# Kernel tuning notes

Measured on AMD Instinct MI355X. Metric: run time of the kernel, lower is better.

The kernel has to match this reference:

```python
import jax, jax.numpy as jnp
import numpy as np
from jax import lax

# config (matches init_kwargs)
NUM_CLASSES = 10
SCORE_THRESH = 0.05
TOPK = 1000
DET_PER_IMG = 100
NMS_SCORE = 0.3
NMS_SIGMA = 0.5
IMG_H, IMG_W = 800.0, 1333.0
IOU_SUPPRESS = 0.8
BBOX_XFORM_CLIP = float(np.log(1000.0 / 16.0))
EPS = 1e-7


def setup_inputs() -> dict:
    key = jax.random.key(0)
    k1, k2, k3 = jax.random.split(key, 3)
    B, A, C = 8, 200000, NUM_CLASSES
    cls_logits = jax.random.normal(k1, (B, A, C), dtype=jnp.float32)
    bbox_regression = 0.5 * jax.random.normal(k2, (B, A, 4), dtype=jnp.float32)
    # plausible anchors: random centers + sizes inside the image, xyxy format
    u = jax.random.uniform(k3, (A, 6), dtype=jnp.float32)
    cx = u[:, 0] * IMG_W
    cy = u[:, 1] * IMG_H
    w = 16.0 + u[:, 2] * 200.0
    h = 16.0 + u[:, 3] * 200.0
    anchors = jnp.stack([cx - 0.5 * w, cy - 0.5 * h, cx + 0.5 * w, cy + 0.5 * h], axis=-1)
    return {"cls_logits": cls_logits, "bbox_regression": bbox_regression, "anchors": anchors}


def _decode(rel, anc):
    # torchvision BoxCoder.decode_single, weights (1,1,1,1). rel, anc: [K,4] xyxy anchors
    wa = anc[:, 2] - anc[:, 0]
    ha = anc[:, 3] - anc[:, 1]
    cxa = anc[:, 0] + 0.5 * wa
    cya = anc[:, 1] + 0.5 * ha
    dx, dy = rel[:, 0], rel[:, 1]
    dw = jnp.minimum(rel[:, 2], BBOX_XFORM_CLIP)
    dh = jnp.minimum(rel[:, 3], BBOX_XFORM_CLIP)
    cx = dx * wa + cxa
    cy = dy * ha + cya
    w = jnp.exp(dw) * wa
    h = jnp.exp(dh) * ha
    boxes = jnp.stack([cx - 0.5 * w, cy - 0.5 * h, cx + 0.5 * w, cy + 0.5 * h], axis=-1)
    # clip_boxes_to_image
    x = jnp.clip(boxes[:, 0::2], 0.0, IMG_W)
    y = jnp.clip(boxes[:, 1::2], 0.0, IMG_H)
    return jnp.stack([x[:, 0], y[:, 0], x[:, 1], y[:, 1]], axis=-1)


def _iou_one(box, boxes):
    # box [4] vs boxes [K,4] -> [K]
    lt = jnp.maximum(box[:2], boxes[:, :2])
    rb = jnp.minimum(box[2:], boxes[:, 2:])
    wh = jnp.clip(rb - lt, 0.0)
    inter = wh[:, 0] * wh[:, 1]
    a1 = (box[2] - box[0]) * (box[3] - box[1])
    a2 = (boxes[:, 2] - boxes[:, 0]) * (boxes[:, 3] - boxes[:, 1])
    return inter / (a1 + a2 - inter + EPS)


def _postprocess_one(logits, rel, anchors):
    # logits [A,C], rel [A,4], anchors [A,4]
    probs = jax.nn.sigmoid(logits)
    scores_all = jnp.max(probs, axis=-1)               # [A]
    labels_all = jnp.argmax(probs, axis=-1)            # [A]
    scores_all = jnp.where(scores_all > SCORE_THRESH, scores_all, 0.0)
    top_scores, top_idx = lax.top_k(scores_all, TOPK)  # [K]
    labels = labels_all[top_idx]
    boxes = _decode(rel[top_idx], anchors[top_idx])    # [K,4]

    K = TOPK
    # --- batched gaussian soft-NMS (same-label decay only) ---
    def soft_step(carry, _):
        sc, out = carry
        i = jnp.argmax(sc)
        s = sc[i]
        out = out.at[i].set(jnp.maximum(s, 0.0))
        ious = _iou_one(boxes[i], boxes)
        decay = jnp.where(labels == labels[i], jnp.exp(-(ious ** 2) / NMS_SIGMA), 1.0)
        sc = (sc * decay).at[i].set(-1.0)
        return (sc, out), None
    (_, decayed), _ = lax.scan(soft_step, (top_scores, jnp.zeros_like(top_scores)), None, length=K)
    keep = decayed > NMS_SCORE

    # --- sort by decayed score desc, greedy hard suppression at IoU>0.8 ---
    order = jnp.argsort(-decayed)
    b = boxes[order]
    s = decayed[order]
    l = labels[order]
    alive0 = keep[order]
    idxs = jnp.arange(K)

    def greedy_step(alive, i):
        ious = _iou_one(b[i], b)
        suppress = (ious > IOU_SUPPRESS) & (idxs > i)
        alive = jnp.where(alive[i], alive & ~suppress, alive)
        return alive, None
    alive, _ = lax.scan(greedy_step, alive0, idxs)

    final_scores = jnp.where(alive, s, -1.0)
    out_scores, out_i = lax.top_k(final_scores, DET_PER_IMG)  # preserves desc order of survivors
    return b[out_i], out_scores, l[out_i]


def reference(cls_logits, bbox_regression, anchors):
    boxes, scores, labels = jax.vmap(_postprocess_one, in_axes=(0, 0, None))(
        cls_logits, bbox_regression, anchors)
    return boxes, scores, labels  # [B,D,4], [B,D], [B,D] (score -1 = padding)
```

## Files before the change

kernel.cpp:

```cpp
#include <hip/hip_runtime.h>
#include <math.h>

#define NCLS 10
#define TOPK 1000
#define DETS 100
#define CANDMAX 4096
#define SLOTS 16
#define ACTK 256
#define TILE 256

#define NB2 256
#define MGATE (-2.9444389791664403f)
#define SEAM 2.2f
#define SCA 30.907200f
#define SCB 41.0f
#define NBLKB 256

__device__ __forceinline__ float sigmoidf_(float x) {
    return 1.0f / (1.0f + expf(-x));
}

__device__ __forceinline__ int mbin_(float m) {
    if (!(m > MGATE)) return 0;
    int b;
    if (m > SEAM) { b = 161 + (int)((m - SEAM) * SCB); if (b > 255) b = 255; }
    else          { b = 1 + (int)((m - MGATE) * SCA);  if (b > 160) b = 160; }
    return b;
}

__device__ __forceinline__ float key_score(const unsigned long long* key, int c) {
    return __uint_as_float(~(unsigned)(key[c] >> 32));
}

__device__ __forceinline__ unsigned fkey_(float f) {
    unsigned b = __float_as_uint(f);
    return (b & 0x80000000u) ? ~b : (b | 0x80000000u);
}
__device__ __forceinline__ float funkey_(unsigned k) {
    return __uint_as_float((k & 0x80000000u) ? (k & 0x7FFFFFFFu) : ~k);
}

__device__ __forceinline__ unsigned wave_umax_(unsigned x) {
    unsigned t;
    t = (unsigned)__builtin_amdgcn_update_dpp(0, (int)x, 0x111, 0xF, 0xF, false); x = (x > t) ? x : t;
    t = (unsigned)__builtin_amdgcn_update_dpp(0, (int)x, 0x112, 0xF, 0xF, false); x = (x > t) ? x : t;
    t = (unsigned)__builtin_amdgcn_update_dpp(0, (int)x, 0x114, 0xF, 0xF, false); x = (x > t) ? x : t;
    t = (unsigned)__builtin_amdgcn_update_dpp(0, (int)x, 0x118, 0xF, 0xF, false); x = (x > t) ? x : t;
    t = (unsigned)__builtin_amdgcn_update_dpp(0, (int)x, 0x142, 0xF, 0xF, false); x = (x > t) ? x : t;
    t = (unsigned)__builtin_amdgcn_update_dpp(0, (int)x, 0x143, 0xF, 0xF, false); x = (x > t) ? x : t;
    return (unsigned)__builtin_amdgcn_readlane((int)x, 63);
}

__global__ __launch_bounds__(256) void k_score_bins(const float* __restrict__ logits,
                                                    unsigned char* __restrict__ binc,
                                                    unsigned* hist,
                                                    unsigned* __restrict__ done,
                                                    unsigned* __restrict__ P,
                                                    int A) {
    __shared__ float tilef[TILE * NCLS];
    __shared__ unsigned h[4][NB2];
    __shared__ int s_last;
    int img = blockIdx.y;
    int tid = threadIdx.x;
    for (int i = tid; i < 4 * NB2; i += 256) ((unsigned*)h)[i] = 0;
    __syncthreads();

    const float* base = logits + (size_t)img * A * NCLS;
    unsigned char* bc = binc + (size_t)img * A;
    int rep = tid & 3;

    int ntile = A / TILE;
    for (int tile = blockIdx.x; tile < ntile; tile += NBLKB) {
        const float4* src = (const float4*)(base + (size_t)tile * TILE * NCLS);
        float4 v0 = src[tid];
        float4 v1 = src[256 + tid];
        float4 v2;
        if (tid < 128) v2 = src[512 + tid];
        ((float4*)tilef)[tid] = v0;
        ((float4*)tilef)[256 + tid] = v1;
        if (tid < 128) ((float4*)tilef)[512 + tid] = v2;
        __syncthreads();
        float m = tilef[tid * 10];
#pragma unroll
        for (int c = 1; c < 10; ++c) m = fmaxf(m, tilef[tid * 10 + c]);
        int b = mbin_(m);
        bc[(size_t)tile * TILE + tid] = (unsigned char)b;
        if (b) atomicAdd(&h[rep][b], 1u);
        __syncthreads();
    }
    if (blockIdx.x == 0) {
        for (int a = ntile * TILE + tid; a < A; a += 256) {
            const float* lp2 = base + (size_t)a * NCLS;
            float m = lp2[0];
            for (int c = 1; c < 10; ++c) m = fmaxf(m, lp2[c]);
            int b = mbin_(m);
            bc[a] = (unsigned char)b;
            if (b) atomicAdd(&h[rep][b], 1u);
        }
    }
    __syncthreads();
    for (int i = tid; i < NB2; i += 256) {
        unsigned c = h[0][i] + h[1][i] + h[2][i] + h[3][i];
        if (c) atomicAdd(&hist[(size_t)img * NB2 + i], c);
    }
    __syncthreads();
    if (tid == 0) {
        __threadfence();
        unsigned old = atomicAdd(&done[img], 1u);
        s_last = (old == (unsigned)(NBLKB - 1)) ? 1 : 0;
    }
    __syncthreads();
    if (s_last && tid < 64) {
        int lane = tid;
        unsigned* hh = hist + (size_t)img * NB2;
        unsigned b4[4];
        unsigned s = 0;
#pragma unroll
        for (int j = 0; j < 4; ++j) { b4[j] = atomicAdd(&hh[lane * 4 + j], 0u); s += b4[j]; }
        unsigned suf = s;
#pragma unroll
        for (int d = 1; d < 64; d <<= 1) {
            unsigned o = __shfl_down(suf, d);
            if (lane + d < 64) suf += o;
        }
        unsigned above = __shfl_down(suf, 1);
        if (lane == 63) above = 0;
        if (lane == 0 && suf < (unsigned)TOPK) P[img] = 0u;
        if (above < (unsigned)TOPK && suf >= (unsigned)TOPK) {
            unsigned cum = above;
            for (int j = 3; j >= 0; --j) {
                cum += b4[j];
                if (cum >= (unsigned)TOPK) { P[img] = (unsigned)(lane * 4 + j); break; }
            }
        }
    }
}

__global__ __launch_bounds__(1024) void k_sortnms(const unsigned char* __restrict__ binc,
                                                  const unsigned* __restrict__ P,
                                                  const float* __restrict__ logits,
                                                  const float* __restrict__ rel,
                                                  const float* __restrict__ anch,
                                                  float* __restrict__ out, int A, int B) {
    __shared__ unsigned long long key[CANDMAX];
    __shared__ float s_box[TOPK][4];
    __shared__ int   s_lab[TOPK];
    __shared__ float s_pbox[TOPK][4];
    __shared__ int   s_plab[TOPK];
    __shared__ float s_psc[TOPK];
    __shared__ int   s_alive[TOPK];
    __shared__ unsigned s_n;

    const float CLIPV = 4.135166556742356f;
    const float EPS = 1e-7f;
    const float W_ = 1333.0f, H_ = 800.0f;

    int img = blockIdx.x;
    int tid = threadIdx.x;
    const float* base = logits + (size_t)img * A * NCLS;

    if (tid == 0) s_n = 0;
    __syncthreads();
    {
        unsigned p = P[img];
        unsigned psel = p ? (p - 1u) : 0u;
        const unsigned* b4 = (const unsigned*)(binc + (size_t)img * A);
        int nquad = A >> 2;
        int nq4 = nquad >> 2;
        for (int g = tid; g < nq4; g += 1024) {
            uint4 u = ((const uint4*)b4)[g];
            unsigned ws[4] = {u.x, u.y, u.z, u.w};
#pragma unroll
            for (int w2 = 0; w2 < 4; ++w2) {
                unsigned ub = ws[w2];
#pragma unroll
                for (int j = 0; j < 4; ++j) {
                    unsigned bj = (ub >> (8 * j)) & 0xFFu;
                    if ((psel == 0u) || (bj >= psel)) {
                        unsigned pos = atomicAdd(&s_n, 1u);
                        if (pos < CANDMAX)
                            key[pos] = (unsigned long long)(unsigned)((g * 4 + w2) * 4 + j);
                    }
                }
            }
        }
        for (int q = (nq4 << 2) + tid; q < nquad; q += 1024) {
            unsigned ub = b4[q];
#pragma unroll
            for (int j = 0; j < 4; ++j) {
                unsigned bj = (ub >> (8 * j)) & 0xFFu;
                if ((psel == 0u) || (bj >= psel)) {
                    unsigned pos = atomicAdd(&s_n, 1u);
                    if (pos < CANDMAX)
                        key[pos] = (unsigned long long)(unsigned)(q * 4 + j);
                }
            }
        }
        for (int a = (nquad << 2) + tid; a < A; a += 1024) {
            unsigned bj = binc[(size_t)img * A + a];
            if ((psel == 0u) || (bj >= psel)) {
                unsigned pos = atomicAdd(&s_n, 1u);
                if (pos < CANDMAX)
                    key[pos] = (unsigned long long)(unsigned)a;
            }
        }
    }
    __syncthreads();
    unsigned n = s_n;
    if (n > CANDMAX) n = CANDMAX;
    int L = (n <= 1024) ? 1024 : (n <= 2048) ? 2048 : CANDMAX;

    for (int t2 = tid; t2 < (int)n; t2 += 1024) {
        unsigned a = (unsigned)key[t2];
        const float* lp = base + (size_t)a * NCLS;
        float m = lp[0];
#pragma unroll
        for (int c = 1; c < 10; ++c) m = fmaxf(m, lp[c]);
        float sc = sigmoidf_(m);
        sc = (sc > 0.05f) ? sc : 0.0f;
        unsigned bits = __float_as_uint(sc);
        key[t2] = ((unsigned long long)(~bits) << 32) | a;
    }
    for (int i = (int)n + tid; i < CANDMAX; i += 1024) key[i] = ~0ull;
    __syncthreads();

    for (int k = 2; k <= L; k <<= 1) {
        for (int j = k >> 1; j > 0; j >>= 1) {
            for (int i = tid; i < L; i += 1024) {
                int l = i ^ j;
                if (l > i) {
                    unsigned long long va = key[i], vb = key[l];
                    bool up = ((i & k) == 0);
                    if (up ? (va > vb) : (va < vb)) { key[i] = vb; key[l] = va; }
                }
            }
            __syncthreads();
        }
    }

    if (tid < TOPK) {
        unsigned long long ik = key[tid];
        unsigned ai = (unsigned)ik;
        if (ai >= (unsigned)A) ai = 0;
        const float* lp = base + (size_t)ai * NCLS;
        float best = sigmoidf_(lp[0]); int lbb = 0;
#pragma unroll
        for (int cc = 1; cc < NCLS; ++cc) {
            float v = sigmoidf_(lp[cc]);
            if (v > best) { best = v; lbb = cc; }
        }
        const float* rp = rel + ((size_t)img * A + ai) * 4;
        const float* ap = anch + (size_t)ai * 4;
        float a0 = ap[0], a1 = ap[1], a2 = ap[2], a3 = ap[3];
        float wa = a2 - a0, ha = a3 - a1;
        float cxa = a0 + 0.5f * wa, cya = a1 + 0.5f * ha;
        float dx = rp[0], dy = rp[1];
        float dw = fminf(rp[2], CLIPV), dh = fminf(rp[3], CLIPV);
        float cx = dx * wa + cxa, cy = dy * ha + cya;
        float w = expf(dw) * wa, h = expf(dh) * ha;
        s_box[tid][0] = fminf(fmaxf(cx - 0.5f * w, 0.0f), W_);
        s_box[tid][1] = fminf(fmaxf(cy - 0.5f * h, 0.0f), H_);
        s_box[tid][2] = fminf(fmaxf(cx + 0.5f * w, 0.0f), W_);
        s_box[tid][3] = fminf(fmaxf(cy + 0.5f * h, 0.0f), H_);
        s_lab[tid] = lbb;
    }
    __syncthreads();
    if (tid >= 64) return;
    int lane = tid;

    int M = TOPK;
    int need_full = 0;
    float bound = key_score(key, ACTK);

    {
        float sc[4], x1[4], y1[4], x2[4], y2[4], ar[4];
        int lb[4];
#pragma unroll
        for (int j = 0; j < 4; ++j) {
            int c = lane + (j << 6);
            float4 bb = *(const float4*)&s_box[c][0];
            x1[j] = bb.x; y1[j] = bb.y; x2[j] = bb.z; y2[j] = bb.w;
            ar[j] = (bb.z - bb.x) * (bb.w - bb.y);
            lb[j] = s_lab[c];
            sc[j] = key_score(key, c);
        }

        int nconf = 0, Mf = -1;

        for (int t = 0; t < ACTK; ++t) {
            float bv = sc[0]; int bj = 0;
#pragma unroll
            for (int j = 1; j < 4; ++j)
                if (sc[j] > bv) { bv = sc[j]; bj = j; }
            unsigned mk = fkey_(bv);
            unsigned mx = wave_umax_(mk);
            float pcur = funkey_(mx);

            if (!(pcur >= bound)) { need_full = 1; break; }

            int pick = -1;
#pragma unroll
            for (int jj = 0; jj < 4; ++jj) {
                if (pick < 0) {
                    unsigned long long mj = __ballot(mk == mx && bj == jj);
                    if (mj) pick = (jj << 6) + (__ffsll(mj) - 1);
                }
            }

            float psc = fmaxf(pcur, 0.0f);
            float4 pb = *(const float4*)&s_box[pick][0];
            int plab_ = s_lab[pick];
            if (lane == 0) {
                *(float4*)&s_pbox[t][0] = pb;
                s_plab[t] = plab_;
                s_psc[t] = psc;
            }

            float4 qb[4]; int ga[4];
#pragma unroll
            for (int k = 0; k < 4; ++k) {
                int p = lane + (k << 6);
                int pc2 = (p < t) ? p : 0;
                qb[k] = *(const float4*)&s_pbox[pc2][0];
                ga[k] = (p < t) ? s_alive[pc2] : 0;
            }

            float wax = (pb.z - pb.x) * (pb.w - pb.y);
#pragma unroll
            for (int j = 0; j < 4; ++j) {
                float lx2 = fmaxf(pb.x, x1[j]), ly2 = fmaxf(pb.y, y1[j]);
                float rx2 = fminf(pb.z, x2[j]), ry2 = fminf(pb.w, y2[j]);
                float iw2 = fmaxf(rx2 - lx2, 0.0f), ih2 = fmaxf(ry2 - ly2, 0.0f);
                float inter2 = iw2 * ih2;
                bool hot = (inter2 > 0.0f) && (lb[j] == plab_);
                if (__ballot(hot) != 0ull) {
                    float iou2 = inter2 / (wax + ar[j] - inter2 + EPS);
                    float ie = (lb[j] == plab_) ? iou2 : 0.0f;
                    sc[j] *= expf(-(ie * ie) / 0.5f);
                }
            }
#pragma unroll
            for (int j = 0; j < 4; ++j)
                if (lane + (j << 6) == pick) sc[j] = -1.0f;

            bool sup = false;
#pragma unroll
            for (int k = 0; k < 4; ++k) {
                if (ga[k]) {
                    float lx = fmaxf(pb.x, qb[k].x), ly = fmaxf(pb.y, qb[k].y);
                    float rx = fminf(pb.z, qb[k].z), ry = fminf(pb.w, qb[k].w);
                    float iw = fmaxf(rx - lx, 0.0f), ih = fmaxf(ry - ly, 0.0f);
                    float inter = iw * ih;
                    float qa = (qb[k].z - qb[k].x) * (qb[k].w - qb[k].y);
                    float iou = inter / (wax + qa - inter + EPS);
                    sup = sup || (iou > 0.8f);
                }
            }
            bool alive = (psc > 0.3f) && (__ballot(sup) == 0ull);
            if (lane == 0) s_alive[t] = alive ? 1 : 0;
            nconf += alive ? 1 : 0;
            if (nconf >= DETS) { Mf = t + 1; break; }
        }
        if (!need_full) {
            if (Mf < 0) need_full = 1;
            else M = Mf;
        }
    }

    if (need_full) {
        float sc[SLOTS], x1[SLOTS], y1[SLOTS], x2[SLOTS], y2[SLOTS], ar[SLOTS];
        int lb[SLOTS];
#pragma unroll
        for (int j = 0; j < SLOTS; ++j) {
            int c = lane + (j << 6);
            if (c < TOPK) {
                float4 bb = *(const float4*)&s_box[c][0];
                x1[j] = bb.x; y1[j] = bb.y; x2[j] = bb.z; y2[j] = bb.w;
                ar[j] = (bb.z - bb.x) * (bb.w - bb.y);
                lb[j] = s_lab[c];
                sc[j] = key_score(key, c);
            } else {
                sc[j] = -2.0f; lb[j] = -1;
                x1[j] = y1[j] = x2[j] = y2[j] = ar[j] = 0.0f;
            }
        }
        unsigned long long aw = 0;
        if (lane < 15) aw = ~0ull;
        else if (lane == 15) aw = (1ull << (TOPK - 15 * 64)) - 1;
        int f = 0, nconf = 0;
        M = TOPK;
        for (int t = 0; t < TOPK; ++t) {
            int fp = (f < TOPK) ? f : 0;
            float4 fb = *(const float4*)&s_box[fp][0];
            int flab = s_lab[fp];
            int fs = f >> 6;
            float v = sc[0];
#pragma unroll
            for (int j = 1; j < SLOTS; ++j) if (fs == j) v = sc[j];
            float cf = __shfl(v, f & 63);
            float lm = sc[0];
#pragma unroll
            for (int j = 1; j < SLOTS; ++j) lm = fmaxf(lm, sc[j]);
            int pick; float pcur; float4 pb; int plab_;
            unsigned long long bb2 = __ballot(lm > cf);
            if (bb2 == 0) {
                pick = f; pcur = cf; pb = fb; plab_ = flab;
            } else {
                float bv = sc[0]; int bi = lane;
#pragma unroll
                for (int j = 1; j < SLOTS; ++j) {
                    int e = lane + (j << 6);
                    if (sc[j] > bv) { bv = sc[j]; bi = e; }
                }
#pragma unroll
                for (int d = 32; d; d >>= 1) {
                    float ov = __shfl_xor(bv, d);
                    int oi = __shfl_xor(bi, d);
                    if (ov > bv || (ov == bv && oi < bi)) { bv = ov; bi = oi; }
                }
                pick = bi; pcur = bv;
                pb = *(const float4*)&s_box[pick][0];
                plab_ = s_lab[pick];
            }
            float psc = fmaxf(pcur, 0.0f);
            if (lane == 0) {
                *(float4*)&s_pbox[t][0] = pb;
                s_plab[t] = plab_;
                s_psc[t] = psc;
            }
            bool alive = (psc > 0.3f);
            if (alive && t > 0) {
                float pa = (pb.z - pb.x) * (pb.w - pb.y);
                int kprev = ((t - 1) >> 6) + 1;
                bool sup = false;
                for (int k = 0; k < kprev; ++k) {
                    int p = lane + (k << 6);
                    int pc = (p < t) ? p : 0;
                    float4 qb = *(const float4*)&s_pbox[pc][0];
                    int ga = s_alive[pc];
                    if (p < t && ga) {
                        float lx = fmaxf(pb.x, qb.x), ly = fmaxf(pb.y, qb.y);
                        float rx = fminf(pb.z, qb.z), ry = fminf(pb.w, qb.w);
                        float iw = fmaxf(rx - lx, 0.0f), ih = fmaxf(ry - ly, 0.0f);
                        float inter = iw * ih;
                        float qa = (qb.z - qb.x) * (qb.w - qb.y);
                        float iou = inter / (pa + qa - inter + EPS);
                        sup = sup || (iou > 0.8f);
                    }
                }
                alive = (__ballot(sup) == 0ull);
            }
            if (lane == 0) s_alive[t] = alive ? 1 : 0;
            nconf += alive ? 1 : 0;
            if (nconf >= DETS) { M = t + 1; break; }
            float wax = (pb.z - pb.x) * (pb.w - pb.y);
#pragma unroll
            for (int j = 0; j < SLOTS; ++j) {
                float lx2 = fmaxf(pb.x, x1[j]), ly2 = fmaxf(pb.y, y1[j]);
                float rx2 = fminf(pb.z, x2[j]), ry2 = fminf(pb.w, y2[j]);
                float iw2 = fmaxf(rx2 - lx2, 0.0f), ih2 = fmaxf(ry2 - ly2, 0.0f);
                float inter2 = iw2 * ih2;
                bool hot = (inter2 > 0.0f) && (lb[j] == plab_);
                if (__ballot(hot) != 0ull) {
                    float iou2 = inter2 / (wax + ar[j] - inter2 + EPS);
                    float ie = (lb[j] == plab_) ? iou2 : 0.0f;
                    sc[j] *= expf(-(ie * ie) / 0.5f);
                }
            }
#pragma unroll
            for (int j = 0; j < SLOTS; ++j)
                if (lane + (j << 6) == pick) sc[j] = -1.0f;
            if (lane == (pick >> 6)) aw &= ~(1ull << (pick & 63));
            if (pick == f) {
                int fw = f >> 6;
                unsigned long long w2 = __shfl(aw, fw);
                while (w2 == 0ull && fw < 15) { ++fw; w2 = __shfl(aw, fw); }
                f = (w2 == 0ull) ? TOPK : (fw << 6) + (__ffsll(w2) - 1);
            }
        }
    }

    float* out_boxes  = out;
    float* out_scores = out + (size_t)B * DETS * 4;
    float* out_labels = out + (size_t)B * DETS * 5;
    int kmax = (M + 63) >> 6;
    int base2 = 0;
    for (int k = 0; k < kmax; ++k) {
        int p = lane + (k << 6);
        bool av = (p < M) && (s_alive[p] != 0);
        unsigned long long mask = __ballot(av);
        int slot = base2 + (int)__popcll(mask & ((1ull << lane) - 1ull));
        if (av && slot < DETS) {
            float4 pb = *(const float4*)&s_pbox[p][0];
            float* ob = out_boxes + ((size_t)img * DETS + slot) * 4;
            ob[0] = pb.x; ob[1] = pb.y; ob[2] = pb.z; ob[3] = pb.w;
            out_scores[img * DETS + slot] = s_psc[p];
            out_labels[img * DETS + slot] = (float)s_plab[p];
        }
        base2 += (int)__popcll(mask);
    }
    if (base2 < DETS) {
        int dbase = 0;
        for (int k = 0; k < kmax; ++k) {
            int p = lane + (k << 6);
            bool dd = (p < M) && (s_alive[p] == 0);
            unsigned long long mask = __ballot(dd);
            int slot = base2 + dbase + (int)__popcll(mask & ((1ull << lane) - 1ull));
            if (dd && slot < DETS) {
                float4 pb = *(const float4*)&s_pbox[p][0];
                float* ob = out_boxes + ((size_t)img * DETS + slot) * 4;
                ob[0] = pb.x; ob[1] = pb.y; ob[2] = pb.z; ob[3] = pb.w;
                out_scores[img * DETS + slot] = -1.0f;
                out_labels[img * DETS + slot] = (float)s_plab[p];
            }
            dbase += (int)__popcll(mask);
        }
    }
}

extern "C" void kernel_launch(void* const* d_in, const int* in_sizes, int n_in,
                              void* d_out, int out_size, void* d_ws, size_t ws_size,
                              hipStream_t stream) {
    const float* logits = (const float*)d_in[0];
    const float* rel = (const float*)d_in[1];
    const float* anch = (const float*)d_in[2];
    float* out = (float*)d_out;

    int A = in_sizes[2] / 4;
    int B = in_sizes[0] / (A * NCLS);

    char* w = (char*)d_ws;
    unsigned* hist = (unsigned*)w;           w += (size_t)B * NB2 * 4;
    unsigned* done = (unsigned*)w;           w += (size_t)B * 4;
    size_t zbytes = (size_t)(w - (char*)d_ws);
    unsigned* P = (unsigned*)w;              w += (size_t)B * 4;
    unsigned char* binc = (unsigned char*)w;

    hipMemsetAsync(d_ws, 0, zbytes, stream);

    dim3 g1(NBLKB, (unsigned)B);
    k_score_bins<<<g1, 256, 0, stream>>>(logits, binc, hist, done, P, A);
    k_sortnms<<<B, 1024, 0, stream>>>(binc, P, logits, rel, anch, out, A, B);
}
```

Baseline: 226.6 us.

## Drop LDS tiling in score-bin pass and skip intra-wave bitonic barriers

```diff
diff --git a/kernel.cpp b/kernel.cpp
--- a/kernel.cpp
+++ b/kernel.cpp
@@ -7,7 +7,6 @@
 #define CANDMAX 4096
 #define SLOTS 16
 #define ACTK 256
-#define TILE 256
 
 #define NB2 256
 #define MGATE (-2.9444389791664403f)
@@ -57,7 +56,6 @@
                                                     unsigned* __restrict__ done,
                                                     unsigned* __restrict__ P,
                                                     int A) {
-    __shared__ float tilef[TILE * NCLS];
     __shared__ unsigned h[4][NB2];
     __shared__ int s_last;
     int img = blockIdx.y;
@@ -69,27 +67,26 @@
     unsigned char* bc = binc + (size_t)img * A;
     int rep = tid & 3;
 
-    int ntile = A / TILE;
-    for (int tile = blockIdx.x; tile < ntile; tile += NBLKB) {
-        const float4* src = (const float4*)(base + (size_t)tile * TILE * NCLS);
-        float4 v0 = src[tid];
-        float4 v1 = src[256 + tid];
-        float4 v2;
-        if (tid < 128) v2 = src[512 + tid];
-        ((float4*)tilef)[tid] = v0;
-        ((float4*)tilef)[256 + tid] = v1;
-        if (tid < 128) ((float4*)tilef)[512 + tid] = v2;
-        __syncthreads();
-        float m = tilef[tid * 10];
-#pragma unroll
-        for (int c = 1; c < 10; ++c) m = fmaxf(m, tilef[tid * 10 + c]);
-        int b = mbin_(m);
-        bc[(size_t)tile * TILE + tid] = (unsigned char)b;
-        if (b) atomicAdd(&h[rep][b], 1u);
-        __syncthreads();
+    int nquad = A >> 2;
+    for (int q = blockIdx.x * 256 + tid; q < nquad; q += NBLKB * 256) {
+        const float4* lp = (const float4*)(base + (size_t)q * 40);
+        float f[40];
+#pragma unroll
+        for (int i = 0; i < 10; ++i) ((float4*)f)[i] = lp[i];
+        unsigned ub = 0;
+#pragma unroll
+        for (int j = 0; j < 4; ++j) {
+            float m = f[10 * j];
+#pragma unroll
+            for (int c = 1; c < 10; ++c) m = fmaxf(m, f[10 * j + c]);
+            int b = mbin_(m);
+            ub |= ((unsigned)b) << (8 * j);
+            if (b) atomicAdd(&h[rep][b], 1u);
+        }
+        *(unsigned*)(bc + (size_t)q * 4) = ub;
     }
     if (blockIdx.x == 0) {
-        for (int a = ntile * TILE + tid; a < A; a += 256) {
+        for (int a = (nquad << 2) + tid; a < A; a += 256) {
             const float* lp2 = base + (size_t)a * NCLS;
             float m = lp2[0];
             for (int c = 1; c < 10; ++c) m = fmaxf(m, lp2[c]);
@@ -224,19 +221,26 @@
     for (int i = (int)n + tid; i < CANDMAX; i += 1024) key[i] = ~0ull;
     __syncthreads();
 
-    for (int k = 2; k <= L; k <<= 1) {
-        for (int j = k >> 1; j > 0; j >>= 1) {
-            for (int i = tid; i < L; i += 1024) {
-                int l = i ^ j;
-                if (l > i) {
-                    unsigned long long va = key[i], vb = key[l];
-                    bool up = ((i & k) == 0);
-                    if (up ? (va > vb) : (va < vb)) { key[i] = vb; key[l] = va; }
-                }
-            }
-            __syncthreads();
-        }
-    }
+    {
+        bool prev_cross = false;
+        for (int k = 2; k <= L; k <<= 1) {
+            for (int j = k >> 1; j > 0; j >>= 1) {
+                bool cross = (j >= 64);
+                if (cross || prev_cross) __syncthreads();
+                else asm volatile("" ::: "memory");
+                for (int i = tid; i < L; i += 1024) {
+                    int l = i ^ j;
+                    if (l > i) {
+                        unsigned long long va = key[i], vb = key[l];
+                        bool up = ((i & k) == 0);
+                        if (up ? (va > vb) : (va < vb)) { key[i] = vb; key[l] = va; }
+                    }
+                }
+                prev_cross = cross;
+            }
+        }
+    }
+    __syncthreads();
 
     if (tid < TOPK) {
         unsigned long long ik = key[tid];
```

After: 238.0 us. 5.0% more time.
